# Kernel optimization log

Hardware: AMD Instinct MI355X
Metric: run time of the kernel (lower is better)

Reference implementation:

```python
import jax, jax.numpy as jnp
import numpy as np

NEG_BIG = -9e15


def setup_inputs() -> dict:
    key = jax.random.key(0)
    k1, k2, k3, k4 = jax.random.split(key, 4)
    B, N, Din, Dout, Hh = 4, 2048, 256, 64, 8
    H = jax.random.normal(k1, (B, N, Din), dtype=jnp.float32)
    adj = jax.random.randint(k2, (B, N, N), 0, 2, dtype=jnp.int32)
    # xavier-uniform-like scale for W [heads, Din, Dout] and a [heads, 2*Dout]
    gain = float(np.sqrt(2.0))  # relu gain
    wb = gain * np.sqrt(6.0 / (Din + Dout))
    ab = gain * np.sqrt(6.0 / (2 * Dout + 1))
    W = jax.random.uniform(k3, (Hh, Din, Dout), jnp.float32, -wb, wb)
    a = jax.random.uniform(k4, (Hh, 2 * Dout), jnp.float32, -ab, ab)
    return {"H": H, "adj": adj, "W": W, "a": a}


def reference(H, adj, W, a):
    # H: [B,N,Din], adj: [B,N,N], W: [h,Din,Dout], a: [h,2*Dout]
    Dout = W.shape[-1]
    Wh = jnp.einsum('bnd,hde->bhne', H, W)          # [B,h,N,Dout]
    a1, a2 = a[:, :Dout], a[:, Dout:]               # [h,Dout] each
    # e_ij = a1 . Wh_i + a2 . Wh_j  (avoids NxNx2D concat blowup)
    f1 = jnp.einsum('bhne,he->bhn', Wh, a1)
    f2 = jnp.einsum('bhne,he->bhn', Wh, a2)
    e = f1[:, :, :, None] + f2[:, :, None, :]        # [B,h,N,N]
    mask = (adj != 0)[:, None, :, :]                 # [B,1,N,N]
    e = jnp.where(mask, e, jnp.asarray(NEG_BIG, e.dtype))
    alpha = jax.nn.softmax(e, axis=-1)               # [B,h,N,N] (dropout=eval no-op)
    h_prime = jnp.einsum('bhnm,bhme->bhne', alpha, Wh)  # [B,h,N,Dout]
    B, h, N, _ = h_prime.shape
    multi = jnp.transpose(h_prime, (0, 2, 1, 3)).reshape(B, N, h * Dout)  # concat heads
    return jax.nn.relu(multi), alpha
```

## Files before the change

kernel.cpp:

```cpp
#include <hip/hip_runtime.h>

#define B_  4
#define N_  2048
#define DIN 256
#define DOUT 64
#define HH  8
#define CH  256

typedef short s8v __attribute__((ext_vector_type(8)));
typedef float f4v __attribute__((ext_vector_type(4)));

__device__ inline unsigned short bfb(float x) {
  return __builtin_bit_cast(unsigned short, (__bf16)x);
}

__global__ __launch_bounds__(256) void k_wh_f2(
    const float* __restrict__ H, const float* __restrict__ W,
    const float* __restrict__ a, unsigned short* __restrict__ Wht,
    float* __restrict__ f2) {
  __shared__ __align__(16) float hs[16][DIN];
  __shared__ __align__(16) float ows[DOUT][20];
  const int t = threadIdx.x, w = t >> 6, lane = t & 63;
  const int q = lane >> 4, g = lane & 15;
  const int bh = blockIdx.x >> 7;
  const int tile = blockIdx.x & 127;
  const int b = bh >> 3, h = bh & 7;
  const int n0 = tile * 16;

  const float* Hbase = H + ((size_t)(b * N_ + n0)) * DIN;
#pragma unroll
  for (int j = 0; j < 4; ++j) {
    int idx = j * 256 + t;
    int row = idx >> 6, c4 = idx & 63;
    float4 v = *reinterpret_cast<const float4*>(Hbase + (size_t)row * DIN + c4 * 4);
    *reinterpret_cast<float4*>(&hs[row][c4 * 4]) = v;
  }
  __syncthreads();

  const float* Wp = W + (size_t)h * DIN * DOUT;
  const float4 a2v = *reinterpret_cast<const float4*>(a + h * (2 * DOUT) + DOUT + 4 * g);

  float4 acc[4];
#pragma unroll
  for (int r = 0; r < 4; ++r) acc[r] = make_float4(0.f, 0.f, 0.f, 0.f);

#pragma unroll 4
  for (int d0 = 0; d0 < DIN; d0 += 4) {
    const float4 wv = *reinterpret_cast<const float4*>(Wp + (size_t)(d0 + q) * DOUT + 4 * g);
#pragma unroll
    for (int r = 0; r < 4; ++r) {
      const float hv = hs[w * 4 + r][d0 + q];
      acc[r].x += hv * wv.x; acc[r].y += hv * wv.y;
      acc[r].z += hv * wv.z; acc[r].w += hv * wv.w;
    }
  }

#pragma unroll
  for (int r = 0; r < 4; ++r) {
    float4 v = acc[r];
#pragma unroll
    for (int off = 16; off <= 32; off <<= 1) {
      v.x += __shfl_xor(v.x, off, 64);
      v.y += __shfl_xor(v.y, off, 64);
      v.z += __shfl_xor(v.z, off, 64);
      v.w += __shfl_xor(v.w, off, 64);
    }
    const int n = n0 + w * 4 + r;
    if (q == 0) {
      ows[4 * g + 0][w * 4 + r] = v.x;
      ows[4 * g + 1][w * 4 + r] = v.y;
      ows[4 * g + 2][w * 4 + r] = v.z;
      ows[4 * g + 3][w * 4 + r] = v.w;
    }
    float fr = v.x * a2v.x + v.y * a2v.y + v.z * a2v.z + v.w * a2v.w;
    fr += __shfl_xor(fr, 1, 64);
    fr += __shfl_xor(fr, 2, 64);
    fr += __shfl_xor(fr, 4, 64);
    fr += __shfl_xor(fr, 8, 64);
    if (lane == 0) f2[(size_t)bh * N_ + n] = fr;
  }
  __syncthreads();

  {
    const int e = t >> 2, quad = t & 3;
    const int seg = tile >> 1, half = tile & 1;
    float4 f = *reinterpret_cast<const float4*>(&ows[e][quad * 4]);
    ushort4 pkv;
    pkv.x = bfb(f.x); pkv.y = bfb(f.y); pkv.z = bfb(f.z); pkv.w = bfb(f.w);
    *reinterpret_cast<ushort4*>(Wht + (size_t)bh * (DOUT * N_) +
                                ((size_t)seg * 64 + e) * 32 + half * 16 + quad * 4) = pkv;
  }
}

__global__ __launch_bounds__(256) void k_ef2(const float* __restrict__ f2,
                                             float* __restrict__ Ef2) {
  __shared__ float red[256];
  const int bh = blockIdx.x;
  const int t = threadIdx.x;
  const float* src = f2 + (size_t)bh * N_;
  float v[8];
  float mx = -1e30f;
#pragma unroll
  for (int j = 0; j < 8; ++j) {
    v[j] = src[t + j * 256];
    mx = fmaxf(mx, v[j]);
  }
  red[t] = mx;
  __syncthreads();
  for (int s = 128; s > 0; s >>= 1) {
    if (t < s) red[t] = fmaxf(red[t], red[t + s]);
    __syncthreads();
  }
  mx = red[0];
  float* dst = Ef2 + (size_t)bh * N_;
#pragma unroll
  for (int j = 0; j < 8; ++j) dst[t + j * 256] = __expf(v[j] - mx);
}

__global__ __launch_bounds__(256) void k_pack(const int* __restrict__ adj,
                                              unsigned long long* __restrict__ bitsG) {
  __shared__ unsigned long long lb[16][32];
  const int t = threadIdx.x, w = t >> 6, lane = t & 63;
  const int b = blockIdx.x >> 7;
  const int n0 = (blockIdx.x & 127) * 16;
  for (int nl = 0; nl < 16; ++nl) {
    const int* arow = adj + ((size_t)(b * N_ + n0 + nl)) * N_;
#pragma unroll
    for (int i = 0; i < 8; ++i) {
      unsigned long long msk = __ballot(arow[w * 512 + i * 64 + lane] != 0);
      if (lane == 0) lb[nl][w * 8 + i] = msk;
    }
  }
  __syncthreads();
  reinterpret_cast<uint4*>(bitsG + (size_t)blockIdx.x * 512)[t] =
      reinterpret_cast<const uint4*>(lb)[t];
}

__global__ __launch_bounds__(256, 4) void k_main(
    const unsigned long long* __restrict__ bitsG, const float* __restrict__ Ef2,
    const unsigned short* __restrict__ WhtG, float* __restrict__ out0,
    float* __restrict__ alpha) {
  __shared__ __align__(16) float ef2s[N_];
  __shared__ __align__(16) unsigned long long bits[16][32];
  __shared__ float ivs[16];
  __shared__ float eas[16];

  const int t = threadIdx.x, w = t >> 6, lane = t & 63;
  const int gr = lane >> 4;
  const int gc = lane & 15;
  const int wg = (blockIdx.x & 7) * 512 + (blockIdx.x >> 3);
  const int bh = wg >> 7;
  const int tile = wg & 127;
  const int b = bh >> 3, h = bh & 7;
  const int n0 = tile * 16;
  const int r = 4 * w + gr;
  const float invN = 1.f / (float)N_;

  reinterpret_cast<uint4*>(&bits[0][0])[t] =
      reinterpret_cast<const uint4*>(bitsG + ((size_t)(b * 128 + tile)) * 512)[t];
  {
    const float4* src = reinterpret_cast<const float4*>(Ef2 + (size_t)bh * N_);
    float4* dst = reinterpret_cast<float4*>(ef2s);
    dst[t] = src[t];
    dst[t + 256] = src[t + 256];
  }
  __syncthreads();

  {
    float s0 = 0.f, s1 = 0.f, s2 = 0.f, s3 = 0.f;
#pragma unroll 4
    for (int k = 0; k < 32; ++k) {
      const float ef = ef2s[k * 64 + lane];
      const unsigned long long w0 = bits[4 * w + 0][k];
      const unsigned long long w1 = bits[4 * w + 1][k];
      const unsigned long long w2 = bits[4 * w + 2][k];
      const unsigned long long w3 = bits[4 * w + 3][k];
      s0 += ((w0 >> lane) & 1ull) ? ef : 0.f;
      s1 += ((w1 >> lane) & 1ull) ? ef : 0.f;
      s2 += ((w2 >> lane) & 1ull) ? ef : 0.f;
      s3 += ((w3 >> lane) & 1ull) ? ef : 0.f;
    }
#pragma unroll
    for (int off = 32; off > 0; off >>= 1) {
      s0 += __shfl_xor(s0, off, 64);
      s1 += __shfl_xor(s1, off, 64);
      s2 += __shfl_xor(s2, off, 64);
      s3 += __shfl_xor(s3, off, 64);
    }
    if (lane == 0) {
      float sv[4] = {s0, s1, s2, s3};
#pragma unroll
      for (int rr = 0; rr < 4; ++rr) {
        const bool emp = (sv[rr] == 0.f);
        ivs[4 * w + rr] = emp ? 0.f : 1.f / sv[rr];
        eas[4 * w + rr] = emp ? invN : 0.f;
      }
    }
  }
  __syncthreads();

  const float ivR = ivs[r], eaR = eas[r];
  const float ivA = ivs[gc], eaA = eas[gc];
  const unsigned* bitsU = reinterpret_cast<const unsigned*>(&bits[0][0]);

  const char* WhtB = reinterpret_cast<const char*>(WhtG + (size_t)bh * (DOUT * N_));
  float* alphaRow = alpha + ((size_t)bh * N_ + (size_t)(n0 + r)) * N_;
  f4v acc = {0.f, 0.f, 0.f, 0.f};

  for (int mc = 0; mc < N_; mc += CH) {
    uint4 bfrag[8];
#pragma unroll
    for (int f = 0; f < 8; ++f) {
      bfrag[f] = *reinterpret_cast<const uint4*>(
          WhtB + (((size_t)((mc >> 5) + f) * 64 + 16 * w + gc) * 32 + gr * 8) * 2);
    }

#pragma unroll
    for (int j4 = 0; j4 < 4; ++j4) {
      const unsigned long long word = bits[r][(mc >> 6) + j4];
      const unsigned nib = (unsigned)(word >> (gc * 4)) & 0xFu;
      const float4 ev = *reinterpret_cast<const float4*>(&ef2s[mc + j4 * 64 + gc * 4]);
      f4v av4;
      av4[0] = ((nib & 1u) ? ev.x * ivR : 0.f) + eaR;
      av4[1] = ((nib & 2u) ? ev.y * ivR : 0.f) + eaR;
      av4[2] = ((nib & 4u) ? ev.z * ivR : 0.f) + eaR;
      av4[3] = ((nib & 8u) ? ev.w * ivR : 0.f) + eaR;
      __builtin_nontemporal_store(
          av4, reinterpret_cast<f4v*>(alphaRow + mc + j4 * 64 + gc * 4));
    }

#pragma unroll
    for (int f = 0; f < 8; ++f) {
      const unsigned u32w = bitsU[gc * 64 + (mc >> 5) + f];
      const unsigned byte = (u32w >> (gr * 8)) & 0xFFu;
      const float4 e0 = *reinterpret_cast<const float4*>(&ef2s[mc + f * 32 + gr * 8]);
      const float4 e1 = *reinterpret_cast<const float4*>(&ef2s[mc + f * 32 + gr * 8 + 4]);
      union { unsigned short u[8]; s8v v; } ap;
      ap.u[0] = bfb(((byte & 1u) ? e0.x * ivA : 0.f) + eaA);
      ap.u[1] = bfb(((byte & 2u) ? e0.y * ivA : 0.f) + eaA);
      ap.u[2] = bfb(((byte & 4u) ? e0.z * ivA : 0.f) + eaA);
      ap.u[3] = bfb(((byte & 8u) ? e0.w * ivA : 0.f) + eaA);
      ap.u[4] = bfb(((byte & 16u) ? e1.x * ivA : 0.f) + eaA);
      ap.u[5] = bfb(((byte & 32u) ? e1.y * ivA : 0.f) + eaA);
      ap.u[6] = bfb(((byte & 64u) ? e1.z * ivA : 0.f) + eaA);
      ap.u[7] = bfb(((byte & 128u) ? e1.w * ivA : 0.f) + eaA);
      acc = __builtin_amdgcn_mfma_f32_16x16x32_bf16(
          ap.v, __builtin_bit_cast(s8v, bfrag[f]), acc, 0, 0, 0);
    }
  }

  {
    float* op = out0 + ((size_t)(b * N_ + n0 + gr * 4)) * (HH * DOUT) +
                h * DOUT + 16 * w + gc;
#pragma unroll
    for (int j = 0; j < 4; ++j) {
      op[(size_t)j * (HH * DOUT)] = fmaxf(acc[j], 0.f);
    }
  }
}

extern "C" void kernel_launch(void* const* d_in, const int* in_sizes, int n_in,
                              void* d_out, int out_size, void* d_ws,
                              size_t ws_size, hipStream_t stream) {
  const float* H = (const float*)d_in[0];
  const int* adj = (const int*)d_in[1];
  const float* W = (const float*)d_in[2];
  const float* a = (const float*)d_in[3];

  float* out = (float*)d_out;
  float* out0 = out;
  float* alpha = out + (size_t)B_ * N_ * HH * DOUT;

  unsigned short* Wht = (unsigned short*)d_ws;
  float* f2 = (float*)(Wht + (size_t)B_ * HH * DOUT * N_);
  float* Ef2 = f2 + (size_t)B_ * HH * N_;
  unsigned long long* bitsG = (unsigned long long*)(Ef2 + (size_t)B_ * HH * N_);

  k_wh_f2<<<B_ * HH * (N_ / 16), 256, 0, stream>>>(H, W, a, Wht, f2);
  k_ef2<<<B_ * HH, 256, 0, stream>>>(f2, Ef2);
  k_pack<<<B_ * (N_ / 16), 256, 0, stream>>>(adj, bitsG);
  k_main<<<B_ * HH * (N_ / 16), 256, 0, stream>>>(bitsG, Ef2, Wht, out0, alpha);
}
```

Before: 205.5 us.

## Fold softmax numerators into scaled Wh and binarize the MFMA A operand

```diff
diff --git a/kernel.cpp b/kernel.cpp
--- a/kernel.cpp
+++ b/kernel.cpp
@@ -16,8 +16,9 @@
 
 __global__ __launch_bounds__(256) void k_wh_f2(
     const float* __restrict__ H, const float* __restrict__ W,
-    const float* __restrict__ a, unsigned short* __restrict__ Wht,
-    float* __restrict__ f2) {
+    const float* __restrict__ a, const int* __restrict__ adj,
+    unsigned short* __restrict__ Wht, float* __restrict__ f2,
+    unsigned long long* __restrict__ bitsG) {
   __shared__ __align__(16) float hs[16][DIN];
   __shared__ __align__(16) float ows[DOUT][20];
   const int t = threadIdx.x, w = t >> 6, lane = t & 63;
@@ -27,6 +28,22 @@
   const int b = bh >> 3, h = bh & 7;
   const int n0 = tile * 16;
 
+  {
+    const int rl = w >> 1, part = w & 1;
+    const int nrow = n0 + 2 * h + rl;
+    const int* arow = adj + ((size_t)b * N_ + nrow) * N_ + part * 1024;
+    int av[16];
+#pragma unroll
+    for (int i = 0; i < 16; ++i) av[i] = arow[i * 64 + lane];
+    unsigned long long* bout =
+        bitsG + ((size_t)(b * 128 + tile)) * 512 + (2 * h + rl) * 32 + part * 16;
+#pragma unroll
+    for (int i = 0; i < 16; ++i) {
+      unsigned long long msk = __ballot(av[i] != 0);
+      if (lane == 0) bout[i] = msk;
+    }
+  }
+
   const float* Hbase = H + ((size_t)(b * N_ + n0)) * DIN;
 #pragma unroll
   for (int j = 0; j < 4; ++j) {
@@ -117,23 +134,31 @@
   for (int j = 0; j < 8; ++j) dst[t + j * 256] = __expf(v[j] - mx);
 }
 
-__global__ __launch_bounds__(256) void k_pack(const int* __restrict__ adj,
-                                              unsigned long long* __restrict__ bitsG) {
-  __shared__ unsigned long long lb[16][32];
-  const int t = threadIdx.x, w = t >> 6, lane = t & 63;
-  const int b = blockIdx.x >> 7;
-  const int n0 = (blockIdx.x & 127) * 16;
-  for (int nl = 0; nl < 16; ++nl) {
-    const int* arow = adj + ((size_t)(b * N_ + n0 + nl)) * N_;
-#pragma unroll
-    for (int i = 0; i < 8; ++i) {
-      unsigned long long msk = __ballot(arow[w * 512 + i * 64 + lane] != 0);
-      if (lane == 0) lb[nl][w * 8 + i] = msk;
-    }
-  }
-  __syncthreads();
-  reinterpret_cast<uint4*>(bitsG + (size_t)blockIdx.x * 512)[t] =
-      reinterpret_cast<const uint4*>(lb)[t];
+__global__ __launch_bounds__(256) void k_scale(const float* __restrict__ Ef2,
+                                               unsigned short* __restrict__ Wht) {
+  __shared__ float efl[32];
+  const int t = threadIdx.x;
+  const int bh = blockIdx.x >> 6;
+  const int seg = blockIdx.x & 63;
+  if (t < 8) {
+    *reinterpret_cast<float4*>(&efl[t * 4]) =
+        *reinterpret_cast<const float4*>(Ef2 + (size_t)bh * N_ + seg * 32 + t * 4);
+  }
+  __syncthreads();
+  unsigned* base = reinterpret_cast<unsigned*>(Wht) + (size_t)bh * 65536 + seg * 1024;
+  uint4 v = *reinterpret_cast<uint4*>(base + t * 4);
+  unsigned rr[4] = {v.x, v.y, v.z, v.w};
+#pragma unroll
+  for (int k2 = 0; k2 < 4; ++k2) {
+    const int mlo = ((t * 4 + k2) * 2) & 31;
+    const unsigned u = rr[k2];
+    float lo = __builtin_bit_cast(float, u << 16);
+    float hi = __builtin_bit_cast(float, u & 0xFFFF0000u);
+    lo *= efl[mlo];
+    hi *= efl[mlo + 1];
+    rr[k2] = ((unsigned)bfb(lo)) | (((unsigned)bfb(hi)) << 16);
+  }
+  *reinterpret_cast<uint4*>(base + t * 4) = make_uint4(rr[0], rr[1], rr[2], rr[3]);
 }
 
 __global__ __launch_bounds__(256, 4) void k_main(
@@ -200,7 +225,6 @@
   __syncthreads();
 
   const float ivR = ivs[r], eaR = eas[r];
-  const float ivA = ivs[gc], eaA = eas[gc];
   const unsigned* bitsU = reinterpret_cast<const unsigned*>(&bits[0][0]);
 
   const char* WhtB = reinterpret_cast<const char*>(WhtG + (size_t)bh * (DOUT * N_));
@@ -233,28 +257,43 @@
     for (int f = 0; f < 8; ++f) {
       const unsigned u32w = bitsU[gc * 64 + (mc >> 5) + f];
       const unsigned byte = (u32w >> (gr * 8)) & 0xFFu;
-      const float4 e0 = *reinterpret_cast<const float4*>(&ef2s[mc + f * 32 + gr * 8]);
-      const float4 e1 = *reinterpret_cast<const float4*>(&ef2s[mc + f * 32 + gr * 8 + 4]);
-      union { unsigned short u[8]; s8v v; } ap;
-      ap.u[0] = bfb(((byte & 1u) ? e0.x * ivA : 0.f) + eaA);
-      ap.u[1] = bfb(((byte & 2u) ? e0.y * ivA : 0.f) + eaA);
-      ap.u[2] = bfb(((byte & 4u) ? e0.z * ivA : 0.f) + eaA);
-      ap.u[3] = bfb(((byte & 8u) ? e0.w * ivA : 0.f) + eaA);
-      ap.u[4] = bfb(((byte & 16u) ? e1.x * ivA : 0.f) + eaA);
-      ap.u[5] = bfb(((byte & 32u) ? e1.y * ivA : 0.f) + eaA);
-      ap.u[6] = bfb(((byte & 64u) ? e1.z * ivA : 0.f) + eaA);
-      ap.u[7] = bfb(((byte & 128u) ? e1.w * ivA : 0.f) + eaA);
+      const unsigned lo4 = ((byte & 0xFu) * 0x00204081u) & 0x01010101u;
+      const unsigned hi4 = ((byte >> 4) * 0x00204081u) & 0x01010101u;
+      union { unsigned u32[4]; s8v v; } ap;
+      ap.u32[0] = (unsigned)__mul24((int)__builtin_amdgcn_perm(0u, lo4, 0x0C010C00u), 0x3F80);
+      ap.u32[1] = (unsigned)__mul24((int)__builtin_amdgcn_perm(0u, lo4, 0x0C030C02u), 0x3F80);
+      ap.u32[2] = (unsigned)__mul24((int)__builtin_amdgcn_perm(0u, hi4, 0x0C010C00u), 0x3F80);
+      ap.u32[3] = (unsigned)__mul24((int)__builtin_amdgcn_perm(0u, hi4, 0x0C030C02u), 0x3F80);
       acc = __builtin_amdgcn_mfma_f32_16x16x32_bf16(
           ap.v, __builtin_bit_cast(s8v, bfrag[f]), acc, 0, 0, 0);
     }
   }
 
-  {
-    float* op = out0 + ((size_t)(b * N_ + n0 + gr * 4)) * (HH * DOUT) +
-                h * DOUT + 16 * w + gc;
-#pragma unroll
+  bool anyEmp = false;
+#pragma unroll
+  for (int rr = 0; rr < 16; ++rr) anyEmp |= (eas[rr] != 0.f);
+
+  float* op = out0 + ((size_t)(b * N_ + n0 + gr * 4)) * (HH * DOUT) +
+              h * DOUT + 16 * w + gc;
+#pragma unroll
+  for (int j = 0; j < 4; ++j) {
+    const float sc = ivs[gr * 4 + j];
+    op[(size_t)j * (HH * DOUT)] = fmaxf(acc[j] * sc, 0.f);
+  }
+
+  if (anyEmp) {
+    const unsigned short* WhtU = reinterpret_cast<const unsigned short*>(WhtB);
     for (int j = 0; j < 4; ++j) {
-      op[(size_t)j * (HH * DOUT)] = fmaxf(acc[j], 0.f);
+      if (eas[gr * 4 + j] != 0.f) {
+        const int e = 16 * w + gc;
+        float sum = 0.f;
+        for (int m = 0; m < N_; ++m) {
+          const unsigned short us = WhtU[((size_t)(m >> 5) * 64 + e) * 32 + (m & 31)];
+          const float whe = __builtin_bit_cast(float, (unsigned)us << 16);
+          sum += whe / ef2s[m];
+        }
+        op[(size_t)j * (HH * DOUT)] = fmaxf(sum * invN, 0.f);
+      }
     }
   }
 }
@@ -276,8 +315,8 @@
   float* Ef2 = f2 + (size_t)B_ * HH * N_;
   unsigned long long* bitsG = (unsigned long long*)(Ef2 + (size_t)B_ * HH * N_);
 
-  k_wh_f2<<<B_ * HH * (N_ / 16), 256, 0, stream>>>(H, W, a, Wht, f2);
+  k_wh_f2<<<B_ * HH * (N_ / 16), 256, 0, stream>>>(H, W, a, adj, Wht, f2, bitsG);
   k_ef2<<<B_ * HH, 256, 0, stream>>>(f2, Ef2);
-  k_pack<<<B_ * (N_ / 16), 256, 0, stream>>>(adj, bitsG);
+  k_scale<<<B_ * HH * (N_ / 32), 256, 0, stream>>>(Ef2, Wht);
   k_main<<<B_ * HH * (N_ / 16), 256, 0, stream>>>(bitsG, Ef2, Wht, out0, alpha);
 }
```

Result: faster. 171.3 us (-16.6%).
